# Kernel tuning notes

Hardware: AMD Instinct MI355X
Metric: run time of the kernel (lower is better)

The kernel has to match this reference:

```python
import jax, jax.numpy as jnp
import numpy as np

B, IB, H, W = 32, 103, 256, 256
P, RB, DIM, DEPTH = 16, 8, 192, 3
KS, KP, TOPK, NC = 24, 24, 2, 9
FFH = 2 * DIM  # max(64, int(dim*2)) = 384
TAU = 0.07 + 1e-08


def ln(x, w, b, eps=1e-5):
    m = x.mean(-1, keepdims=True)
    v = ((x - m) ** 2).mean(-1, keepdims=True)
    return (x - m) / jnp.sqrt(v + eps) * w + b


def setup_inputs() -> dict:
    key = jax.random.key(0)
    keys = iter(jax.random.split(key, 40))
    nrm = lambda shape, s=0.02: jax.random.normal(next(keys), shape, jnp.float32) * s
    return {
        "x": jax.random.normal(next(keys), (B, IB, H, W), jnp.float32),
        "band_w": nrm((RB, IB), 0.05), "band_b": jnp.zeros((RB,), jnp.float32),
        "dw_w": nrm((RB, P, P), 0.05), "pw_w": nrm((DIM, RB), 0.1),
        "pe_ln_w": jnp.ones((DIM,), jnp.float32), "pe_ln_b": jnp.zeros((DIM,), jnp.float32),
        "spec_proto": nrm((KS, RB)), "spat_proto": nrm((KP, DIM)),
        "r1_w": nrm((DIM, 128), 0.05), "r1_b": jnp.zeros((128,), jnp.float32),
        "r2_w": nrm((128, KS + KP), 0.05), "r2_b": jnp.zeros((KS + KP,), jnp.float32),
        "key_w": nrm((RB + DIM, DIM), 0.05),
        "pos_bias": jnp.zeros((1, 1, DIM), jnp.float32),
        "blk_ln_w": jnp.ones((DEPTH, DIM), jnp.float32), "blk_ln_b": jnp.zeros((DEPTH, DIM), jnp.float32),
        "blk_q_w": nrm((DEPTH, DIM, DIM), 0.05), "blk_v_w": nrm((DEPTH, DIM, DIM), 0.05),
        "blk_f1_w": nrm((DEPTH, DIM, FFH), 0.05), "blk_f1_b": jnp.zeros((DEPTH, FFH), jnp.float32),
        "blk_f2_w": nrm((DEPTH, FFH, DIM), 0.05), "blk_f2_b": jnp.zeros((DEPTH, DIM), jnp.float32),
        "blk_g1": jnp.full((DEPTH, DIM), 0.01, jnp.float32), "blk_g2": jnp.full((DEPTH, DIM), 0.01, jnp.float32),
        "fin_ln_w": jnp.ones((DIM,), jnp.float32), "fin_ln_b": jnp.zeros((DIM,), jnp.float32),
        "head_w": nrm((DIM, NC), 0.01), "head_b": jnp.zeros((NC,), jnp.float32),
    }


def _forward(x, band_w, band_b, dw_w, pw_w, pe_ln_w, pe_ln_b, spec_proto, spat_proto,
             r1_w, r1_b, r2_w, r2_b, key_w, pos_bias,
             blk_ln_w, blk_ln_b, blk_q_w, blk_v_w, blk_f1_w, blk_f1_b, blk_f2_w, blk_f2_b,
             blk_g1, blk_g2, fin_ln_w, fin_ln_b, head_w, head_b):
    # 1x1 band reduction conv: (B,103,H,W) -> (B,8,H,W)
    x_red = jnp.einsum('bchw,oc->bohw', x, band_w) + band_b[None, :, None, None]
    Bn, C, Hh, Ww = x_red.shape
    hp, wp = Hh // P, Ww // P
    # depthwise conv, kernel==stride==P -> non-overlapping patches
    patches = x_red.reshape(Bn, C, hp, P, wp, P)
    dw = jnp.einsum('bcipjq,cpq->bcij', patches, dw_w)        # (B,RB,hp,wp)
    pw = jnp.einsum('bcij,dc->bdij', dw, pw_w)                # (B,DIM,hp,wp)
    tok = pw.reshape(Bn, DIM, hp * wp).transpose(0, 2, 1)     # (B,N,DIM)
    tok = ln(tok, pe_ln_w, pe_ln_b)
    # router -> topk -> softmax gate -> gather prototypes -> weighted sum
    h = jax.nn.gelu(tok @ r1_w + r1_b, approximate=False)
    rlogits = h @ r2_w + r2_b                                 # (B,N,KS+KP)
    s_vals, s_idx = jax.lax.top_k(rlogits[..., :KS], TOPK)
    p_vals, p_idx = jax.lax.top_k(rlogits[..., KS:], TOPK)
    w_s = jax.nn.softmax(s_vals / TAU, axis=-1)               # (B,N,TOPK)
    w_p = jax.nn.softmax(p_vals / TAU, axis=-1)
    spec_mixed = (spec_proto[s_idx] * w_s[..., None]).sum(2)  # (B,N,RB)
    spat_mixed = (spat_proto[p_idx] * w_p[..., None]).sum(2)  # (B,N,DIM)
    keys_t = jnp.concatenate([spec_mixed, spat_mixed], -1) @ key_w + pos_bias  # (B,N,DIM)
    # linear-attention blocks
    xb = tok
    for i in range(DEPTH):
        xn = ln(xb, blk_ln_w[i], blk_ln_b[i])
        q = xn @ blk_q_w[i]
        v = xn @ blk_v_w[i]
        q_s = jax.nn.softmax(q, axis=-1)
        KV = jnp.einsum('bnc,bnd->bcd', keys_t, v)            # (B,C,C)
        out = jnp.einsum('bnc,bcd->bnd', q_s, KV)             # (B,N,C)
        xb = xb + out * blk_g1[i]
        xn2 = ln(xb, blk_ln_w[i], blk_ln_b[i])
        ff = jax.nn.gelu(xn2 @ blk_f1_w[i] + blk_f1_b[i], approximate=False) @ blk_f2_w[i] + blk_f2_b[i]
        xb = xb + ff * blk_g2[i]
    feat = ln(xb.mean(1), fin_ln_w, fin_ln_b)                 # (B,DIM)
    return feat @ head_w + head_b                             # (B,NC)


def reference(x, band_w, band_b, dw_w, pw_w, pe_ln_w, pe_ln_b, spec_proto, spat_proto,
              r1_w, r1_b, r2_w, r2_b, key_w, pos_bias,
              blk_ln_w, blk_ln_b, blk_q_w, blk_v_w, blk_f1_w, blk_f1_b, blk_f2_w, blk_f2_b,
              blk_g1, blk_g2, fin_ln_w, fin_ln_b, head_w, head_b):
    return _forward(x, band_w, band_b, dw_w, pw_w, pe_ln_w, pe_ln_b, spec_proto, spat_proto,
                    r1_w, r1_b, r2_w, r2_b, key_w, pos_bias,
                    blk_ln_w, blk_ln_b, blk_q_w, blk_v_w, blk_f1_w, blk_f1_b, blk_f2_w, blk_f2_b,
                    blk_g1, blk_g2, fin_ln_w, fin_ln_b, head_w, head_b)
```

## Files before the change

### kernel.cpp

```cpp
#include <hip/hip_runtime.h>
#include <math.h>


typedef __attribute__((ext_vector_type(8))) short bf16x8;
typedef __attribute__((ext_vector_type(4))) float f32x4;

__device__ __forceinline__ float wsum64(float v) {
#pragma unroll
  for (int o = 32; o > 0; o >>= 1) v += __shfl_xor(v, o, 64);
  return v;
}
__device__ __forceinline__ float sum16(float v) {
#pragma unroll
  for (int o = 8; o > 0; o >>= 1) v += __shfl_xor(v, o, 64);
  return v;
}
__device__ __forceinline__ float max16(float v) {
#pragma unroll
  for (int o = 8; o > 0; o >>= 1) v = fmaxf(v, __shfl_xor(v, o, 64));
  return v;
}
__device__ __forceinline__ float gelu_f(float x) {
  return 0.5f * x * (1.0f + erff(x * 0.7071067811865476f));
}
__device__ __forceinline__ ushort f2bf(float f) {
  union { float f; unsigned u; } v;
  v.f = f;
  unsigned r = v.u + 0x7FFFu + ((v.u >> 16) & 1u);
  return (ushort)(r >> 16);
}

__global__ __launch_bounds__(256) void prep_w(
    const float* __restrict__ qw, const float* __restrict__ vw,
    const float* __restrict__ f1w, const float* __restrict__ f2w,
    const float* __restrict__ r1_w, const float* __restrict__ r2_w,
    const float* __restrict__ key_w, const float* __restrict__ band_w,
    ushort* __restrict__ qwT, ushort* __restrict__ vwT,
    ushort* __restrict__ f1T, ushort* __restrict__ f2T,
    ushort* __restrict__ r1T, ushort* __restrict__ r2T,
    ushort* __restrict__ keyT, float* __restrict__ bandT) {
  const int i = blockIdx.x * 256 + threadIdx.x;
  if (i < 110592) {
    const int d = i / 36864, r = i % 36864;
    const int k = r / 192, c = r % 192;
    qwT[d * 36864 + c * 192 + k] = f2bf(qw[i]);
    vwT[d * 36864 + c * 192 + k] = f2bf(vw[i]);
  }
  if (i < 221184) {
    const int d = i / 73728, r = i % 73728;
    const int k = r / 384, j = r % 384;
    f1T[d * 73728 + j * 192 + k] = f2bf(f1w[i]);
    const int k2 = r / 192, j2 = r % 192;
    f2T[d * 73728 + j2 * 384 + k2] = f2bf(f2w[i]);
  }
  if (i < 24576) {
    const int j = i / 192, k = i % 192;
    r1T[i] = f2bf(r1_w[k * 128 + j]);
  }
  if (i < 6144) {
    const int j = i / 128, k = i % 128;
    r2T[i] = f2bf(r2_w[k * 48 + j]);
  }
  if (i < 43008) {
    const int j = i / 224, k = i % 224;
    keyT[i] = (k < 200) ? f2bf(key_w[k * 192 + j]) : (ushort)0;
  }
  if (i < 824) {
    const int ch = i >> 3, c = i & 7;
    bandT[i] = band_w[c * 103 + ch];
  }
}

__global__ __launch_bounds__(512) void k1_band_dw(
    const float* __restrict__ x, const float* __restrict__ bandT,
    const float* __restrict__ band_b, const float* __restrict__ dw_w,
    float* __restrict__ dw_out) {
  const int blk = blockIdx.x;
  const int b = blk >> 4, ip = blk & 15;
  const int t = threadIdx.x;
  const int col4 = t & 63;
  const int j = col4 >> 2;
  const int qb = (col4 & 3) << 2;
  const int p0 = t >> 6;

  float acc[8][8];
#pragma unroll
  for (int e = 0; e < 8; ++e)
#pragma unroll
    for (int c = 0; c < 8; ++c) acc[e][c] = 0.f;

  const f32x4* xp = (const f32x4*)x + (size_t)b * (103 * 16384) + (size_t)ip * 1024;

  auto body = [&](const f32x4 v0, const f32x4 v1, const int ch) {
    const f32x4 wA = *(const f32x4*)&bandT[ch * 8];
    const f32x4 wB = *(const f32x4*)&bandT[ch * 8 + 4];
    const float bw[8] = {wA.x, wA.y, wA.z, wA.w, wB.x, wB.y, wB.z, wB.w};
#pragma unroll
    for (int c = 0; c < 8; ++c) {
      acc[0][c] = fmaf(v0.x, bw[c], acc[0][c]);
      acc[1][c] = fmaf(v0.y, bw[c], acc[1][c]);
      acc[2][c] = fmaf(v0.z, bw[c], acc[2][c]);
      acc[3][c] = fmaf(v0.w, bw[c], acc[3][c]);
      acc[4][c] = fmaf(v1.x, bw[c], acc[4][c]);
      acc[5][c] = fmaf(v1.y, bw[c], acc[5][c]);
      acc[6][c] = fmaf(v1.z, bw[c], acc[6][c]);
      acc[7][c] = fmaf(v1.w, bw[c], acc[7][c]);
    }
  };

  f32x4 p0v = __builtin_nontemporal_load(&xp[t]);
  f32x4 p1v = __builtin_nontemporal_load(&xp[t + 512]);
  f32x4 q0v = __builtin_nontemporal_load(&xp[t + 16384]);
  f32x4 q1v = __builtin_nontemporal_load(&xp[t + 16896]);
#pragma unroll 1
  for (int ch = 0; ch < 100; ch += 2) {
    const f32x4 r0 = __builtin_nontemporal_load(&xp[t + 2 * 16384]);
    const f32x4 r1 = __builtin_nontemporal_load(&xp[t + 2 * 16384 + 512]);
    const f32x4 s0 = __builtin_nontemporal_load(&xp[t + 3 * 16384]);
    const f32x4 s1 = __builtin_nontemporal_load(&xp[t + 3 * 16384 + 512]);
    body(p0v, p1v, ch);
    body(q0v, q1v, ch + 1);
    p0v = r0; p1v = r1; q0v = s0; q1v = s1;
    xp += 2 * 16384;
  }
  const f32x4 u0 = __builtin_nontemporal_load(&xp[t + 2 * 16384]);
  const f32x4 u1 = __builtin_nontemporal_load(&xp[t + 2 * 16384 + 512]);
  body(p0v, p1v, 100);
  body(q0v, q1v, 101);
  body(u0, u1, 102);

  float dwt[8];
#pragma unroll
  for (int c = 0; c < 8; ++c) dwt[c] = 0.f;
#pragma unroll
  for (int e = 0; e < 8; ++e) {
    const int pp = p0 + ((e >> 2) << 3);
    const int qq = qb + (e & 3);
#pragma unroll
    for (int c = 0; c < 8; ++c)
      dwt[c] = fmaf(dw_w[c * 256 + pp * 16 + qq], acc[e][c] + band_b[c], dwt[c]);
  }
#pragma unroll
  for (int c = 0; c < 8; ++c) {
    dwt[c] += __shfl_xor(dwt[c], 1, 64);
    dwt[c] += __shfl_xor(dwt[c], 2, 64);
  }
  __shared__ float part[8][16][8];
  if ((t & 3) == 0) {
#pragma unroll
    for (int c = 0; c < 8; ++c) part[t >> 6][j][c] = dwt[c];
  }
  __syncthreads();
  if (t < 128) {
    const int jj = t >> 3, c = t & 7;
    float s = 0.f;
#pragma unroll
    for (int w = 0; w < 8; ++w) s += part[w][jj][c];
    dw_out[(((size_t)b * 16 + ip) * 16 + jj) * 8 + c] = s;
  }
}

__global__ __launch_bounds__(256) void k2_mfma(
    const float* __restrict__ dw, const float* __restrict__ pw_w,
    const float* __restrict__ pe_ln_w, const float* __restrict__ pe_ln_b,
    const float* __restrict__ spec_proto, const float* __restrict__ spat_proto,
    const ushort* __restrict__ r1T, const float* __restrict__ r1_b,
    const ushort* __restrict__ r2T, const float* __restrict__ r2_b,
    const ushort* __restrict__ keyT, const float* __restrict__ pos_bias,
    float* __restrict__ xb_out, ushort* __restrict__ keysT) {
  const int t = threadIdx.x;
  const int lane = t & 63, wid = t >> 6;
  const int wm = wid >> 1, wn = wid & 1;
  const int l15 = lane & 15, lg4 = lane >> 4;
  const int tok0 = blockIdx.x * 32;
  const int rl = wm * 16 + 4 * lg4;
  const int b = blockIdx.x >> 3;
  const int n0 = (blockIdx.x & 7) * 32;

  __shared__ float dw8s[32][8];
  __shared__ __align__(16) ushort s_xn[32][200];
  __shared__ __align__(16) ushort s_w[192][40];
  __shared__ __align__(16) ushort s_h[32][200];
  __shared__ __align__(16) ushort s_mix[32][232];
  __shared__ float s_rl[32][48];
  __shared__ float topwS[32][4];
  __shared__ int   topiS[32][4];

  dw8s[t >> 3][t & 7] = dw[((size_t)tok0 + (t >> 3)) * 8 + (t & 7)];
  __syncthreads();

#pragma unroll
  for (int half = 0; half < 2; ++half) {
    const int tt = half * 16 + (t >> 4), lg = t & 15;
    float pre[12], sm = 0.f;
#pragma unroll
    for (int m = 0; m < 12; ++m) {
      const int d = lg + 16 * m;
      const f32x4 pa = *(const f32x4*)&pw_w[d * 8];
      const f32x4 pb = *(const f32x4*)&pw_w[d * 8 + 4];
      float p = pa.x * dw8s[tt][0] + pa.y * dw8s[tt][1] + pa.z * dw8s[tt][2] +
                pa.w * dw8s[tt][3] + pb.x * dw8s[tt][4] + pb.y * dw8s[tt][5] +
                pb.z * dw8s[tt][6] + pb.w * dw8s[tt][7];
      pre[m] = p;
      sm += p;
    }
    sm = sum16(sm);
    const float mean = sm * (1.f / 192.f);
    float vv = 0.f;
#pragma unroll
    for (int m = 0; m < 12; ++m) {
      const float d0 = pre[m] - mean;
      vv = fmaf(d0, d0, vv);
    }
    vv = sum16(vv);
    const float inv = rsqrtf(vv * (1.f / 192.f) + 1e-5f);
#pragma unroll
    for (int m = 0; m < 12; ++m) {
      const int d = lg + 16 * m;
      const float xv = (pre[m] - mean) * inv * pe_ln_w[d] + pe_ln_b[d];
      s_xn[tt][d] = f2bf(xv);
      xb_out[((size_t)tok0 + tt) * 192 + d] = xv;
    }
  }
  __syncthreads();

  {
    f32x4 hacc[4];
#pragma unroll
    for (int f = 0; f < 4; ++f) hacc[f] = (f32x4){0.f, 0.f, 0.f, 0.f};
#pragma unroll 1
    for (int ks = 0; ks < 6; ++ks) {
#pragma unroll
      for (int i = 0; i < 2; ++i) {
        const int lin = t + 256 * i;
        const int row = lin >> 2, c8 = (lin & 3) * 8;
        *(uint4*)&s_w[row][c8] = *(const uint4*)&r1T[row * 192 + ks * 32 + c8];
      }
      __syncthreads();
      const bf16x8 a = *(const bf16x8*)&s_xn[wm * 16 + l15][ks * 32 + 8 * lg4];
#pragma unroll
      for (int f = 0; f < 4; ++f) {
        const bf16x8 bb = *(const bf16x8*)&s_w[wn * 64 + 16 * f + l15][8 * lg4];
        hacc[f] = __builtin_amdgcn_mfma_f32_16x16x32_bf16(a, bb, hacc[f], 0, 0, 0);
      }
      __syncthreads();
    }
#pragma unroll
    for (int f = 0; f < 4; ++f) {
      const int col = wn * 64 + 16 * f + l15;
#pragma unroll
      for (int reg = 0; reg < 4; ++reg)
        s_h[rl + reg][col] = f2bf(gelu_f(hacc[f][reg] + r1_b[col]));
    }
  }
  __syncthreads();

  {
    f32x4 racc[2];
    racc[0] = (f32x4){0.f, 0.f, 0.f, 0.f};
    racc[1] = (f32x4){0.f, 0.f, 0.f, 0.f};
#pragma unroll 1
    for (int ks = 0; ks < 4; ++ks) {
      if (t < 192) {
        const int row = t >> 2, c8 = (t & 3) * 8;
        *(uint4*)&s_w[row][c8] = *(const uint4*)&r2T[row * 128 + ks * 32 + c8];
      }
      __syncthreads();
      const bf16x8 a = *(const bf16x8*)&s_h[wm * 16 + l15][ks * 32 + 8 * lg4];
      if (wn == 0) {
#pragma unroll
        for (int f = 0; f < 2; ++f) {
          const bf16x8 bb = *(const bf16x8*)&s_w[16 * f + l15][8 * lg4];
          racc[f] = __builtin_amdgcn_mfma_f32_16x16x32_bf16(a, bb, racc[f], 0, 0, 0);
        }
      } else {
        const bf16x8 bb = *(const bf16x8*)&s_w[32 + l15][8 * lg4];
        racc[0] = __builtin_amdgcn_mfma_f32_16x16x32_bf16(a, bb, racc[0], 0, 0, 0);
      }
      __syncthreads();
    }
    if (wn == 0) {
#pragma unroll
      for (int f = 0; f < 2; ++f) {
        const int col = 16 * f + l15;
#pragma unroll
        for (int reg = 0; reg < 4; ++reg)
          s_rl[rl + reg][col] = racc[f][reg] + r2_b[col];
      }
    } else {
      const int col = 32 + l15;
#pragma unroll
      for (int reg = 0; reg < 4; ++reg)
        s_rl[rl + reg][col] = racc[0][reg] + r2_b[col];
    }
  }
  __syncthreads();

  if (t < 64) {
    const int tt = t >> 1, half = t & 1;
    const float* base = &s_rl[tt][half * 24];
    float v0 = -1e30f, v1 = -1e30f;
    int i0 = 0, i1 = 0;
    for (int k = 0; k < 24; ++k) {
      const float vv = base[k];
      if (vv > v0) { v1 = v0; i1 = i0; v0 = vv; i0 = k; }
      else if (vv > v1) { v1 = vv; i1 = k; }
    }
    const float tau = (float)(0.07 + 1e-8);
    const float e1 = expf((v1 - v0) / tau);
    const float inv = 1.f / (1.f + e1);
    topwS[tt][half * 2] = inv;
    topwS[tt][half * 2 + 1] = e1 * inv;
    topiS[tt][half * 2] = i0;
    topiS[tt][half * 2 + 1] = i1;
  }
  __syncthreads();

#pragma unroll
  for (int r = 0; r < 28; ++r) {
    const int f = t + 256 * r;
    const int tok = f / 224, c = f % 224;
    float val = 0.f;
    if (c < 8) {
      val = topwS[tok][0] * spec_proto[topiS[tok][0] * 8 + c] +
            topwS[tok][1] * spec_proto[topiS[tok][1] * 8 + c];
    } else if (c < 200) {
      const int cc = c - 8;
      val = topwS[tok][2] * spat_proto[topiS[tok][2] * 192 + cc] +
            topwS[tok][3] * spat_proto[topiS[tok][3] * 192 + cc];
    }
    s_mix[tok][c] = f2bf(val);
  }
  __syncthreads();

  {
    f32x4 kacc[6];
#pragma unroll
    for (int f = 0; f < 6; ++f) kacc[f] = (f32x4){0.f, 0.f, 0.f, 0.f};
#pragma unroll 1
    for (int ks = 0; ks < 7; ++ks) {
#pragma unroll
      for (int i = 0; i < 3; ++i) {
        const int lin = t + 256 * i;
        const int row = lin >> 2, c8 = (lin & 3) * 8;
        *(uint4*)&s_w[row][c8] = *(const uint4*)&keyT[row * 224 + ks * 32 + c8];
      }
      __syncthreads();
      const bf16x8 a = *(const bf16x8*)&s_mix[wm * 16 + l15][ks * 32 + 8 * lg4];
#pragma unroll
      for (int f = 0; f < 6; ++f) {
        const bf16x8 bb = *(const bf16x8*)&s_w[wn * 96 + 16 * f + l15][8 * lg4];
        kacc[f] = __builtin_amdgcn_mfma_f32_16x16x32_bf16(a, bb, kacc[f], 0, 0, 0);
      }
      __syncthreads();
    }
#pragma unroll
    for (int f = 0; f < 6; ++f) {
      const int col = wn * 96 + 16 * f + l15;
#pragma unroll
      for (int reg = 0; reg < 4; ++reg)
        keysT[((size_t)b * 192 + col) * 256 + n0 + rl + reg] =
            f2bf(kacc[f][reg] + pos_bias[col]);
    }
  }
}

__global__ __launch_bounds__(256) void k3a_mfma(
    const float* __restrict__ xb, const float* __restrict__ lnw,
    const float* __restrict__ lnb, const ushort* __restrict__ qwT,
    const ushort* __restrict__ vwT, ushort* __restrict__ qs_bf,
    ushort* __restrict__ vT, int depth) {
  const int t = threadIdx.x;
  const int lane = t & 63, wid = t >> 6;
  const int l15 = lane & 15, lg4 = lane >> 4;
  const int tok0 = blockIdx.x * 16;
  const int b = blockIdx.x >> 4;
  const int n0 = (blockIdx.x & 15) * 16;
  const int rl = 4 * lg4;

  __shared__ __align__(16) char smem[6400 + 15360 + 15360];
  ushort (*s_xn)[200] = (ushort(*)[200])smem;
  ushort (*s_wq)[40] = (ushort(*)[40])(smem + 6400);
  ushort (*s_wv)[40] = (ushort(*)[40])(smem + 6400 + 15360);
  float (*s_q)[196] = (float(*)[196])(smem + 6400);

  const float* lw = lnw + depth * 192;
  const float* lb = lnb + depth * 192;
  {
    const int tt = t >> 4;
    const int lg = t & 15;
    const float* xrow = xb + ((size_t)tok0 + tt) * 192;
    float vals[12], sm = 0.f;
#pragma unroll
    for (int m = 0; m < 12; ++m) {
      vals[m] = xrow[lg + 16 * m];
      sm += vals[m];
    }
    sm = sum16(sm);
    const float mean = sm * (1.f / 192.f);
    float vv = 0.f;
#pragma unroll
    for (int m = 0; m < 12; ++m) {
      const float d0 = vals[m] - mean;
      vv = fmaf(d0, d0, vv);
    }
    vv = sum16(vv);
    const float inv = rsqrtf(vv * (1.f / 192.f) + 1e-5f);
#pragma unroll
    for (int m = 0; m < 12; ++m) {
      const int d = lg + 16 * m;
      s_xn[tt][d] = f2bf((vals[m] - mean) * inv * lw[d] + lb[d]);
    }
  }
  __syncthreads();

  f32x4 aq[3], av[3];
#pragma unroll
  for (int f = 0; f < 3; ++f) {
    aq[f] = (f32x4){0.f, 0.f, 0.f, 0.f};
    av[f] = (f32x4){0.f, 0.f, 0.f, 0.f};
  }
  const ushort* qbase = qwT + depth * 36864;
  const ushort* vbase = vwT + depth * 36864;
#pragma unroll 1
  for (int ks = 0; ks < 6; ++ks) {
#pragma unroll
    for (int i = 0; i < 3; ++i) {
      const int idx = t + 256 * i;
      const int row = idx >> 2, c4 = (idx & 3) * 8;
      *(uint4*)&s_wq[row][c4] = *(const uint4*)&qbase[row * 192 + ks * 32 + c4];
      *(uint4*)&s_wv[row][c4] = *(const uint4*)&vbase[row * 192 + ks * 32 + c4];
    }
    __syncthreads();
    const bf16x8 a = *(const bf16x8*)&s_xn[l15][ks * 32 + 8 * lg4];
#pragma unroll
    for (int f = 0; f < 3; ++f) {
      const bf16x8 bq = *(const bf16x8*)&s_wq[wid * 48 + 16 * f + l15][8 * lg4];
      const bf16x8 bv = *(const bf16x8*)&s_wv[wid * 48 + 16 * f + l15][8 * lg4];
      aq[f] = __builtin_amdgcn_mfma_f32_16x16x32_bf16(a, bq, aq[f], 0, 0, 0);
      av[f] = __builtin_amdgcn_mfma_f32_16x16x32_bf16(a, bv, av[f], 0, 0, 0);
    }
    __syncthreads();
  }

#pragma unroll
  for (int f = 0; f < 3; ++f) {
    const int col = wid * 48 + 16 * f + l15;
#pragma unroll
    for (int reg = 0; reg < 4; ++reg) {
      vT[((size_t)b * 192 + col) * 256 + n0 + rl + reg] = f2bf(av[f][reg]);
      s_q[rl + reg][col] = aq[f][reg];
    }
  }
  __syncthreads();

  {
    const int tt = t >> 4;
    const int lg = t & 15;
    float vals[12], mx = -1e30f;
#pragma unroll
    for (int m = 0; m < 12; ++m) {
      vals[m] = s_q[tt][lg + 16 * m];
      mx = fmaxf(mx, vals[m]);
    }
    mx = max16(mx);
    float s = 0.f;
#pragma unroll
    for (int m = 0; m < 12; ++m) {
      vals[m] = expf(vals[m] - mx);
      s += vals[m];
    }
    s = sum16(s);
    const float inv = 1.f / s;
#pragma unroll
    for (int m = 0; m < 12; ++m)
      qs_bf[((size_t)tok0 + tt) * 192 + lg + 16 * m] = f2bf(vals[m] * inv);
  }
}

__global__ __launch_bounds__(256) void k3b_mfma(
    const ushort* __restrict__ vT, const ushort* __restrict__ keysT,
    ushort* __restrict__ kvT) {
  const int t = threadIdx.x;
  const int lane = t & 63, wid = t >> 6;
  const int l15 = lane & 15, lg4 = lane >> 4;
  const int b = blockIdx.x / 12;
  const int d0 = (blockIdx.x % 12) * 16;
  const int rl = 4 * lg4;

  __shared__ __align__(16) ushort s_a[16][264];
  __shared__ __align__(16) ushort s_w[192][40];

  const ushort* vbase = vT + ((size_t)b * 192 + d0) * 256;
#pragma unroll
  for (int i = 0; i < 2; ++i) {
    const int idx = t + 256 * i;
    const int row = idx >> 5, c8 = (idx & 31) * 8;
    *(uint4*)&s_a[row][c8] = *(const uint4*)&vbase[row * 256 + c8];
  }

  f32x4 acc[3];
#pragma unroll
  for (int f = 0; f < 3; ++f) acc[f] = (f32x4){0.f, 0.f, 0.f, 0.f};
  const ushort* kbase = keysT + (size_t)b * 192 * 256;
#pragma unroll 1
  for (int ks = 0; ks < 8; ++ks) {
#pragma unroll
    for (int i = 0; i < 3; ++i) {
      const int idx = t + 256 * i;
      const int row = idx >> 2, c4 = (idx & 3) * 8;
      *(uint4*)&s_w[row][c4] = *(const uint4*)&kbase[row * 256 + ks * 32 + c4];
    }
    __syncthreads();
    const bf16x8 a = *(const bf16x8*)&s_a[l15][ks * 32 + 8 * lg4];
#pragma unroll
    for (int f = 0; f < 3; ++f) {
      const bf16x8 bb = *(const bf16x8*)&s_w[wid * 48 + 16 * f + l15][8 * lg4];
      acc[f] = __builtin_amdgcn_mfma_f32_16x16x32_bf16(a, bb, acc[f], 0, 0, 0);
    }
    __syncthreads();
  }

#pragma unroll
  for (int f = 0; f < 3; ++f) {
    const int col = wid * 48 + 16 * f + l15;
#pragma unroll
    for (int reg = 0; reg < 4; ++reg)
      kvT[((size_t)b * 192 + d0 + rl + reg) * 192 + col] = f2bf(acc[f][reg]);
  }
}

__global__ __launch_bounds__(256) void k3c_mfma(
    float* __restrict__ xb, const ushort* __restrict__ qs_bf,
    const ushort* __restrict__ kvT, const float* __restrict__ lnw,
    const float* __restrict__ lnb, const ushort* __restrict__ f1T,
    const ushort* __restrict__ f2T, const float* __restrict__ f1b,
    const float* __restrict__ f2b, const float* __restrict__ g1,
    const float* __restrict__ g2, int depth) {
  const int t = threadIdx.x;
  const int lane = t & 63, wid = t >> 6;
  const int l15 = lane & 15, lg4 = lane >> 4;
  const int tok0 = blockIdx.x * 16;
  const int b = blockIdx.x >> 4;
  const int rl = 4 * lg4;

  __shared__ __align__(16) ushort s_a[16][200];
  __shared__ __align__(16) ushort s_w[192][40];
  __shared__ __align__(16) ushort s_ff[16][200];
  __shared__ float s_red[16][8];

#pragma unroll
  for (int i = 0; i < 2; ++i) {
    const int idx = t + 256 * i;
    if (idx < 384) {
      const int row = idx / 24, c8 = (idx % 24) * 8;
      *(uint4*)&s_a[row][c8] =
          *(const uint4*)&qs_bf[((size_t)tok0 + row) * 192 + c8];
    }
  }
  __syncthreads();

  f32x4 o1[3];
#pragma unroll
  for (int f = 0; f < 3; ++f) o1[f] = (f32x4){0.f, 0.f, 0.f, 0.f};
  const ushort* kvb = kvT + (size_t)b * 36864;
#pragma unroll 1
  for (int ks = 0; ks < 6; ++ks) {
#pragma unroll
    for (int i = 0; i < 3; ++i) {
      const int idx = t + 256 * i;
      const int row = idx >> 2, c4 = (idx & 3) * 8;
      *(uint4*)&s_w[row][c4] = *(const uint4*)&kvb[row * 192 + ks * 32 + c4];
    }
    __syncthreads();
    const bf16x8 a = *(const bf16x8*)&s_a[l15][ks * 32 + 8 * lg4];
#pragma unroll
    for (int f = 0; f < 3; ++f) {
      const bf16x8 bb = *(const bf16x8*)&s_w[wid * 48 + 16 * f + l15][8 * lg4];
      o1[f] = __builtin_amdgcn_mfma_f32_16x16x32_bf16(a, bb, o1[f], 0, 0, 0);
    }
    __syncthreads();
  }

  const float* g1p = g1 + depth * 192;
  const float* lw = lnw + depth * 192;
  const float* lb = lnb + depth * 192;
  float xbn[3][4];
  float psum[4] = {0.f, 0.f, 0.f, 0.f}, psq[4] = {0.f, 0.f, 0.f, 0.f};
#pragma unroll
  for (int f = 0; f < 3; ++f) {
    const int col = wid * 48 + 16 * f + l15;
#pragma unroll
    for (int reg = 0; reg < 4; ++reg) {
      const float xv =
          xb[((size_t)tok0 + rl + reg) * 192 + col] + o1[f][reg] * g1p[col];
      xbn[f][reg] = xv;
      psum[reg] += xv;
      psq[reg] = fmaf(xv, xv, psq[reg]);
    }
  }
#pragma unroll
  for (int reg = 0; reg < 4; ++reg) {
#pragma unroll
    for (int o = 8; o > 0; o >>= 1) {
      psum[reg] += __shfl_xor(psum[reg], o, 64);
      psq[reg] += __shfl_xor(psq[reg], o, 64);
    }
  }
  if (l15 == 0) {
#pragma unroll
    for (int reg = 0; reg < 4; ++reg) {
      s_red[rl + reg][wid] = psum[reg];
      s_red[rl + reg][4 + wid] = psq[reg];
    }
  }
  __syncthreads();
  float mean[4], inv[4];
#pragma unroll
  for (int reg = 0; reg < 4; ++reg) {
    const float s = s_red[rl + reg][0] + s_red[rl + reg][1] +
                    s_red[rl + reg][2] + s_red[rl + reg][3];
    const float q = s_red[rl + reg][4] + s_red[rl + reg][5] +
                    s_red[rl + reg][6] + s_red[rl + reg][7];
    mean[reg] = s * (1.f / 192.f);
    const float var = q * (1.f / 192.f) - mean[reg] * mean[reg];
    inv[reg] = rsqrtf(var + 1e-5f);
  }
#pragma unroll
  for (int f = 0; f < 3; ++f) {
    const int col = wid * 48 + 16 * f + l15;
#pragma unroll
    for (int reg = 0; reg < 4; ++reg)
      s_a[rl + reg][col] =
          f2bf((xbn[f][reg] - mean[reg]) * inv[reg] * lw[col] + lb[col]);
  }
  __syncthreads();

  f32x4 o2[3];
#pragma unroll
  for (int f = 0; f < 3; ++f) o2[f] = (f32x4){0.f, 0.f, 0.f, 0.f};
#pragma unroll 1
  for (int h = 0; h < 2; ++h) {
    f32x4 hh[3];
#pragma unroll
    for (int f = 0; f < 3; ++f) hh[f] = (f32x4){0.f, 0.f, 0.f, 0.f};
    const ushort* f1base = f1T + depth * 73728 + h * 36864;
#pragma unroll 1
    for (int ks = 0; ks < 6; ++ks) {
#pragma unroll
      for (int i = 0; i < 3; ++i) {
        const int idx = t + 256 * i;
        const int row = idx >> 2, c4 = (idx & 3) * 8;
        *(uint4*)&s_w[row][c4] = *(const uint4*)&f1base[row * 192 + ks * 32 + c4];
      }
      __syncthreads();
      const bf16x8 a = *(const bf16x8*)&s_a[l15][ks * 32 + 8 * lg4];
#pragma unroll
      for (int f = 0; f < 3; ++f) {
        const bf16x8 bb = *(const bf16x8*)&s_w[wid * 48 + 16 * f + l15][8 * lg4];
        hh[f] = __builtin_amdgcn_mfma_f32_16x16x32_bf16(a, bb, hh[f], 0, 0, 0);
      }
      __syncthreads();
    }
    const float* b1p = f1b + depth * 384 + h * 192;
#pragma unroll
    for (int f = 0; f < 3; ++f) {
      const int col = wid * 48 + 16 * f + l15;
#pragma unroll
      for (int reg = 0; reg < 4; ++reg)
        s_ff[rl + reg][col] = f2bf(gelu_f(hh[f][reg] + b1p[col]));
    }
    __syncthreads();
    const ushort* f2base = f2T + depth * 73728;
#pragma unroll 1
    for (int ks2 = 0; ks2 < 6; ++ks2) {
#pragma unroll
      for (int i = 0; i < 3; ++i) {
        const int idx = t + 256 * i;
        const int row = idx >> 2, c4 = (idx & 3) * 8;
        *(uint4*)&s_w[row][c4] =
            *(const uint4*)&f2base[row * 384 + h * 192 + ks2 * 32 + c4];
      }
      __syncthreads();
      const bf16x8 a = *(const bf16x8*)&s_ff[l15][ks2 * 32 + 8 * lg4];
#pragma unroll
      for (int f = 0; f < 3; ++f) {
        const bf16x8 bb = *(const bf16x8*)&s_w[wid * 48 + 16 * f + l15][8 * lg4];
        o2[f] = __builtin_amdgcn_mfma_f32_16x16x32_bf16(a, bb, o2[f], 0, 0, 0);
      }
      __syncthreads();
    }
  }

  const float* b2p = f2b + depth * 192;
  const float* g2p = g2 + depth * 192;
#pragma unroll
  for (int f = 0; f < 3; ++f) {
    const int col = wid * 48 + 16 * f + l15;
#pragma unroll
    for (int reg = 0; reg < 4; ++reg)
      xb[((size_t)tok0 + rl + reg) * 192 + col] =
          xbn[f][reg] + (o2[f][reg] + b2p[col]) * g2p[col];
  }
}

__global__ __launch_bounds__(192) void k4_head(
    const float* __restrict__ xb, const float* __restrict__ flnw,
    const float* __restrict__ flnb, const float* __restrict__ hw,
    const float* __restrict__ hb, float* __restrict__ out) {
  const int b = blockIdx.x, t = threadIdx.x;
  const int w = t >> 6, lane = t & 63;
  float s = 0.f;
  const float* base = xb + (size_t)b * 256 * 192 + t;
#pragma unroll 4
  for (int n = 0; n < 256; ++n) s += base[n * 192];
  const float feat_pre = s * (1.f / 256.f);
  __shared__ float red[3];
  __shared__ float feat[192];
  float sm = wsum64(feat_pre);
  if (lane == 0) red[w] = sm;
  __syncthreads();
  const float mean = (red[0] + red[1] + red[2]) * (1.f / 192.f);
  __syncthreads();
  const float dd = feat_pre - mean;
  sm = wsum64(dd * dd);
  if (lane == 0) red[w] = sm;
  __syncthreads();
  const float var = (red[0] + red[1] + red[2]) * (1.f / 192.f);
  feat[t] = dd * rsqrtf(var + 1e-5f) * flnw[t] + flnb[t];
  __syncthreads();
  if (t < 9) {
    float a = hb[t];
    for (int d = 0; d < 192; ++d) a = fmaf(feat[d], hw[d * 9 + t], a);
    out[b * 9 + t] = a;
  }
}

extern "C" void kernel_launch(void* const* d_in, const int* in_sizes, int n_in,
                              void* d_out, int out_size, void* d_ws, size_t ws_size,
                              hipStream_t stream) {
  (void)in_sizes; (void)n_in; (void)out_size; (void)ws_size;
  const float* x          = (const float*)d_in[0];
  const float* band_w     = (const float*)d_in[1];
  const float* band_b     = (const float*)d_in[2];
  const float* dw_w       = (const float*)d_in[3];
  const float* pw_w       = (const float*)d_in[4];
  const float* pe_ln_w    = (const float*)d_in[5];
  const float* pe_ln_b    = (const float*)d_in[6];
  const float* spec_proto = (const float*)d_in[7];
  const float* spat_proto = (const float*)d_in[8];
  const float* r1_w       = (const float*)d_in[9];
  const float* r1_b       = (const float*)d_in[10];
  const float* r2_w       = (const float*)d_in[11];
  const float* r2_b       = (const float*)d_in[12];
  const float* key_w      = (const float*)d_in[13];
  const float* pos_bias   = (const float*)d_in[14];
  const float* blk_ln_w   = (const float*)d_in[15];
  const float* blk_ln_b   = (const float*)d_in[16];
  const float* blk_q_w    = (const float*)d_in[17];
  const float* blk_v_w    = (const float*)d_in[18];
  const float* blk_f1_w   = (const float*)d_in[19];
  const float* blk_f1_b   = (const float*)d_in[20];
  const float* blk_f2_w   = (const float*)d_in[21];
  const float* blk_f2_b   = (const float*)d_in[22];
  const float* blk_g1     = (const float*)d_in[23];
  const float* blk_g2     = (const float*)d_in[24];
  const float* fin_ln_w   = (const float*)d_in[25];
  const float* fin_ln_b   = (const float*)d_in[26];
  const float* head_w     = (const float*)d_in[27];
  const float* head_b     = (const float*)d_in[28];

  float* ws    = (float*)d_ws;
  float* dw    = ws;
  float* xbuf  = dw + 65536;
  float* bandT = xbuf + 1572864;
  ushort* ush    = (ushort*)(bandT + 1024);
  ushort* qs_bf  = ush;
  ushort* kvT    = qs_bf + 1572864;
  ushort* keysT  = kvT + 1179648;
  ushort* vT     = keysT + 1572864;
  ushort* qwT    = vT + 1572864;
  ushort* vwT    = qwT + 110592;
  ushort* f1T    = vwT + 110592;
  ushort* f2T    = f1T + 221184;
  ushort* r1T    = f2T + 221184;
  ushort* r2T    = r1T + 24576;
  ushort* keyT   = r2T + 6144;

  prep_w<<<864, 256, 0, stream>>>(blk_q_w, blk_v_w, blk_f1_w, blk_f2_w,
                                  r1_w, r2_w, key_w, band_w,
                                  qwT, vwT, f1T, f2T, r1T, r2T, keyT, bandT);
  k1_band_dw<<<512, 512, 0, stream>>>(x, bandT, band_b, dw_w, dw);
  k2_mfma<<<256, 256, 0, stream>>>(dw, pw_w, pe_ln_w, pe_ln_b, spec_proto,
                                   spat_proto, r1T, r1_b, r2T, r2_b, keyT,
                                   pos_bias, xbuf, keysT);
  for (int d = 0; d < 3; ++d) {
    k3a_mfma<<<512, 256, 0, stream>>>(xbuf, blk_ln_w, blk_ln_b, qwT, vwT,
                                      qs_bf, vT, d);
    k3b_mfma<<<384, 256, 0, stream>>>(vT, keysT, kvT);
    k3c_mfma<<<512, 256, 0, stream>>>(xbuf, qs_bf, kvT, blk_ln_w, blk_ln_b,
                                      f1T, f2T, blk_f1_b, blk_f2_b, blk_g1,
                                      blk_g2, d);
  }
  k4_head<<<32, 192, 0, stream>>>(xbuf, fin_ln_w, fin_ln_b, head_w, head_b,
                                  (float*)d_out);
}
```

Before: 320.6 us.

## Fuse next block's LN+Q/V projection and softmax into FFN kernel epilogue

```diff
diff --git a/kernel.cpp b/kernel.cpp
--- a/kernel.cpp
+++ b/kernel.cpp
@@ -530,24 +530,30 @@
   }
 }
 
-__global__ __launch_bounds__(256) void k3c_mfma(
-    float* __restrict__ xb, const ushort* __restrict__ qs_bf,
+__global__ __launch_bounds__(256) void k3ca_mfma(
+    float* __restrict__ xb, ushort* __restrict__ qs_bf,
     const ushort* __restrict__ kvT, const float* __restrict__ lnw,
     const float* __restrict__ lnb, const ushort* __restrict__ f1T,
     const ushort* __restrict__ f2T, const float* __restrict__ f1b,
     const float* __restrict__ f2b, const float* __restrict__ g1,
-    const float* __restrict__ g2, int depth) {
+    const float* __restrict__ g2, const ushort* __restrict__ qwT,
+    const ushort* __restrict__ vwT, ushort* __restrict__ vT,
+    int depth, int fuse_next) {
   const int t = threadIdx.x;
   const int lane = t & 63, wid = t >> 6;
   const int l15 = lane & 15, lg4 = lane >> 4;
   const int tok0 = blockIdx.x * 16;
   const int b = blockIdx.x >> 4;
+  const int n0 = (blockIdx.x & 15) * 16;
   const int rl = 4 * lg4;
 
-  __shared__ __align__(16) ushort s_a[16][200];
-  __shared__ __align__(16) ushort s_w[192][40];
-  __shared__ __align__(16) ushort s_ff[16][200];
-  __shared__ float s_red[16][8];
+  __shared__ __align__(16) char smem[6400 + 15360 + 15360 + 6400 + 512];
+  ushort (*s_a)[200] = (ushort(*)[200])smem;
+  ushort (*s_w)[40] = (ushort(*)[40])(smem + 6400);
+  ushort (*s_w2)[40] = (ushort(*)[40])(smem + 6400 + 15360);
+  ushort (*s_ff)[200] = (ushort(*)[200])(smem + 6400 + 2 * 15360);
+  float (*s_red)[8] = (float(*)[8])(smem + 6400 + 2 * 15360 + 6400);
+  float (*s_q)[196] = (float(*)[196])(smem + 6400);
 
 #pragma unroll
   for (int i = 0; i < 2; ++i) {
@@ -586,53 +592,57 @@
   const float* lw = lnw + depth * 192;
   const float* lb = lnb + depth * 192;
   float xbn[3][4];
-  float psum[4] = {0.f, 0.f, 0.f, 0.f}, psq[4] = {0.f, 0.f, 0.f, 0.f};
-#pragma unroll
-  for (int f = 0; f < 3; ++f) {
-    const int col = wid * 48 + 16 * f + l15;
+  {
+    float psum[4] = {0.f, 0.f, 0.f, 0.f}, psq[4] = {0.f, 0.f, 0.f, 0.f};
+#pragma unroll
+    for (int f = 0; f < 3; ++f) {
+      const int col = wid * 48 + 16 * f + l15;
+#pragma unroll
+      for (int reg = 0; reg < 4; ++reg) {
+        const float xv =
+            xb[((size_t)tok0 + rl + reg) * 192 + col] + o1[f][reg] * g1p[col];
+        xbn[f][reg] = xv;
+        psum[reg] += xv;
+        psq[reg] = fmaf(xv, xv, psq[reg]);
+      }
+    }
 #pragma unroll
     for (int reg = 0; reg < 4; ++reg) {
-      const float xv =
-          xb[((size_t)tok0 + rl + reg) * 192 + col] + o1[f][reg] * g1p[col];
-      xbn[f][reg] = xv;
-      psum[reg] += xv;
-      psq[reg] = fmaf(xv, xv, psq[reg]);
-    }
-  }
-#pragma unroll
-  for (int reg = 0; reg < 4; ++reg) {
-#pragma unroll
-    for (int o = 8; o > 0; o >>= 1) {
-      psum[reg] += __shfl_xor(psum[reg], o, 64);
-      psq[reg] += __shfl_xor(psq[reg], o, 64);
-    }
-  }
-  if (l15 == 0) {
+#pragma unroll
+      for (int o = 8; o > 0; o >>= 1) {
+        psum[reg] += __shfl_xor(psum[reg], o, 64);
+        psq[reg] += __shfl_xor(psq[reg], o, 64);
+      }
+    }
+    if (l15 == 0) {
+#pragma unroll
+      for (int reg = 0; reg < 4; ++reg) {
+        s_red[rl + reg][wid] = psum[reg];
+        s_red[rl + reg][4 + wid] = psq[reg];
+      }
+    }
+  }
+  __syncthreads();
+  {
+    float mean[4], inv[4];
 #pragma unroll
     for (int reg = 0; reg < 4; ++reg) {
-      s_red[rl + reg][wid] = psum[reg];
-      s_red[rl + reg][4 + wid] = psq[reg];
-    }
-  }
-  __syncthreads();
-  float mean[4], inv[4];
-#pragma unroll
-  for (int reg = 0; reg < 4; ++reg) {
-    const float s = s_red[rl + reg][0] + s_red[rl + reg][1] +
-                    s_red[rl + reg][2] + s_red[rl + reg][3];
-    const float q = s_red[rl + reg][4] + s_red[rl + reg][5] +
-                    s_red[rl + reg][6] + s_red[rl + reg][7];
-    mean[reg] = s * (1.f / 192.f);
-    const float var = q * (1.f / 192.f) - mean[reg] * mean[reg];
-    inv[reg] = rsqrtf(var + 1e-5f);
-  }
-#pragma unroll
-  for (int f = 0; f < 3; ++f) {
-    const int col = wid * 48 + 16 * f + l15;
-#pragma unroll
-    for (int reg = 0; reg < 4; ++reg)
-      s_a[rl + reg][col] =
-          f2bf((xbn[f][reg] - mean[reg]) * inv[reg] * lw[col] + lb[col]);
+      const float s = s_red[rl + reg][0] + s_red[rl + reg][1] +
+                      s_red[rl + reg][2] + s_red[rl + reg][3];
+      const float q = s_red[rl + reg][4] + s_red[rl + reg][5] +
+                      s_red[rl + reg][6] + s_red[rl + reg][7];
+      mean[reg] = s * (1.f / 192.f);
+      const float var = q * (1.f / 192.f) - mean[reg] * mean[reg];
+      inv[reg] = rsqrtf(var + 1e-5f);
+    }
+#pragma unroll
+    for (int f = 0; f < 3; ++f) {
+      const int col = wid * 48 + 16 * f + l15;
+#pragma unroll
+      for (int reg = 0; reg < 4; ++reg)
+        s_a[rl + reg][col] =
+            f2bf((xbn[f][reg] - mean[reg]) * inv[reg] * lw[col] + lb[col]);
+    }
   }
   __syncthreads();
 
@@ -694,13 +704,132 @@
 
   const float* b2p = f2b + depth * 192;
   const float* g2p = g2 + depth * 192;
+  float xfin[3][4];
 #pragma unroll
   for (int f = 0; f < 3; ++f) {
     const int col = wid * 48 + 16 * f + l15;
 #pragma unroll
-    for (int reg = 0; reg < 4; ++reg)
-      xb[((size_t)tok0 + rl + reg) * 192 + col] =
-          xbn[f][reg] + (o2[f][reg] + b2p[col]) * g2p[col];
+    for (int reg = 0; reg < 4; ++reg) {
+      xfin[f][reg] = xbn[f][reg] + (o2[f][reg] + b2p[col]) * g2p[col];
+      xb[((size_t)tok0 + rl + reg) * 192 + col] = xfin[f][reg];
+    }
+  }
+
+  if (!fuse_next) return;
+
+  {
+    float psum[4] = {0.f, 0.f, 0.f, 0.f}, psq[4] = {0.f, 0.f, 0.f, 0.f};
+#pragma unroll
+    for (int f = 0; f < 3; ++f) {
+#pragma unroll
+      for (int reg = 0; reg < 4; ++reg) {
+        psum[reg] += xfin[f][reg];
+        psq[reg] = fmaf(xfin[f][reg], xfin[f][reg], psq[reg]);
+      }
+    }
+#pragma unroll
+    for (int reg = 0; reg < 4; ++reg) {
+#pragma unroll
+      for (int o = 8; o > 0; o >>= 1) {
+        psum[reg] += __shfl_xor(psum[reg], o, 64);
+        psq[reg] += __shfl_xor(psq[reg], o, 64);
+      }
+    }
+    if (l15 == 0) {
+#pragma unroll
+      for (int reg = 0; reg < 4; ++reg) {
+        s_red[rl + reg][wid] = psum[reg];
+        s_red[rl + reg][4 + wid] = psq[reg];
+      }
+    }
+  }
+  __syncthreads();
+  {
+    const float* lw2 = lnw + (depth + 1) * 192;
+    const float* lb2 = lnb + (depth + 1) * 192;
+    float mean[4], inv[4];
+#pragma unroll
+    for (int reg = 0; reg < 4; ++reg) {
+      const float s = s_red[rl + reg][0] + s_red[rl + reg][1] +
+                      s_red[rl + reg][2] + s_red[rl + reg][3];
+      const float q = s_red[rl + reg][4] + s_red[rl + reg][5] +
+                      s_red[rl + reg][6] + s_red[rl + reg][7];
+      mean[reg] = s * (1.f / 192.f);
+      const float var = q * (1.f / 192.f) - mean[reg] * mean[reg];
+      inv[reg] = rsqrtf(var + 1e-5f);
+    }
+#pragma unroll
+    for (int f = 0; f < 3; ++f) {
+      const int col = wid * 48 + 16 * f + l15;
+#pragma unroll
+      for (int reg = 0; reg < 4; ++reg)
+        s_a[rl + reg][col] =
+            f2bf((xfin[f][reg] - mean[reg]) * inv[reg] * lw2[col] + lb2[col]);
+    }
+  }
+  __syncthreads();
+
+  f32x4 aq[3], av[3];
+#pragma unroll
+  for (int f = 0; f < 3; ++f) {
+    aq[f] = (f32x4){0.f, 0.f, 0.f, 0.f};
+    av[f] = (f32x4){0.f, 0.f, 0.f, 0.f};
+  }
+  const ushort* qbase = qwT + (depth + 1) * 36864;
+  const ushort* vbase = vwT + (depth + 1) * 36864;
+#pragma unroll 1
+  for (int ks = 0; ks < 6; ++ks) {
+#pragma unroll
+    for (int i = 0; i < 3; ++i) {
+      const int idx = t + 256 * i;
+      const int row = idx >> 2, c4 = (idx & 3) * 8;
+      *(uint4*)&s_w[row][c4] = *(const uint4*)&qbase[row * 192 + ks * 32 + c4];
+      *(uint4*)&s_w2[row][c4] = *(const uint4*)&vbase[row * 192 + ks * 32 + c4];
+    }
+    __syncthreads();
+    const bf16x8 a = *(const bf16x8*)&s_a[l15][ks * 32 + 8 * lg4];
+#pragma unroll
+    for (int f = 0; f < 3; ++f) {
+      const bf16x8 bq = *(const bf16x8*)&s_w[wid * 48 + 16 * f + l15][8 * lg4];
+      const bf16x8 bv = *(const bf16x8*)&s_w2[wid * 48 + 16 * f + l15][8 * lg4];
+      aq[f] = __builtin_amdgcn_mfma_f32_16x16x32_bf16(a, bq, aq[f], 0, 0, 0);
+      av[f] = __builtin_amdgcn_mfma_f32_16x16x32_bf16(a, bv, av[f], 0, 0, 0);
+    }
+    __syncthreads();
+  }
+
+#pragma unroll
+  for (int f = 0; f < 3; ++f) {
+    const int col = wid * 48 + 16 * f + l15;
+#pragma unroll
+    for (int reg = 0; reg < 4; ++reg) {
+      vT[((size_t)b * 192 + col) * 256 + n0 + rl + reg] = f2bf(av[f][reg]);
+      s_q[rl + reg][col] = aq[f][reg];
+    }
+  }
+  __syncthreads();
+
+  {
+    const int tt = t >> 4;
+    const int lg = t & 15;
+    float vals[12], mx = -1e30f;
+#pragma unroll
+    for (int m = 0; m < 12; ++m) {
+      vals[m] = s_q[tt][lg + 16 * m];
+      mx = fmaxf(mx, vals[m]);
+    }
+    mx = max16(mx);
+    float s = 0.f;
+#pragma unroll
+    for (int m = 0; m < 12; ++m) {
+      vals[m] = expf(vals[m] - mx);
+      s += vals[m];
+    }
+    s = sum16(s);
+    const float inv = 1.f / s;
+#pragma unroll
+    for (int m = 0; m < 12; ++m)
+      qs_bf[((size_t)tok0 + tt) * 192 + lg + 16 * m] = f2bf(vals[m] * inv);
   }
 }
 
@@ -794,13 +923,13 @@
   k2_mfma<<<256, 256, 0, stream>>>(dw, pw_w, pe_ln_w, pe_ln_b, spec_proto,
                                    spat_proto, r1T, r1_b, r2T, r2_b, keyT,
                                    pos_bias, xbuf, keysT);
+  k3a_mfma<<<512, 256, 0, stream>>>(xbuf, blk_ln_w, blk_ln_b, qwT, vwT,
+                                    qs_bf, vT, 0);
   for (int d = 0; d < 3; ++d) {
-    k3a_mfma<<<512, 256, 0, stream>>>(xbuf, blk_ln_w, blk_ln_b, qwT, vwT,
-                                      qs_bf, vT, d);
     k3b_mfma<<<384, 256, 0, stream>>>(vT, keysT, kvT);
-    k3c_mfma<<<512, 256, 0, stream>>>(xbuf, qs_bf, kvT, blk_ln_w, blk_ln_b,
-                                      f1T, f2T, blk_f1_b, blk_f2_b, blk_g1,
-                                      blk_g2, d);
+    k3ca_mfma<<<512, 256, 0, stream>>>(xbuf, qs_bf, kvT, blk_ln_w, blk_ln_b,
+                                       f1T, f2T, blk_f1_b, blk_f2_b, blk_g1,
+                                       blk_g2, qwT, vwT, vT, d, (d < 2) ? 1 : 0);
   }
   k4_head<<<32, 192, 0, stream>>>(xbuf, fin_ln_w, fin_ln_b, head_w, head_b,
                                   (float*)d_out);
```

Result: no change. 316.8 us (-1.2%).
